# Kernel tuning notes

Measured on AMD Instinct MI355X. Metric: run time of the kernel, lower is better.

## Reference

```python
import jax, jax.numpy as jnp
import numpy as np

DIM, HEADS, MLP_HID = 1024, 16, 4096
B, N = 2, 2048
EPS = 1e-5

def setup_inputs() -> dict:
    key = jax.random.key(0)
    ks = jax.random.split(key, 8)
    s = lambda fan_in: 1.0 / np.sqrt(fan_in)
    return {
        "x": jax.random.normal(ks[0], (B, N, DIM), jnp.float32),
        "ln1_w": jnp.ones((DIM,), jnp.float32),
        "ln1_b": jnp.zeros((DIM,), jnp.float32),
        # weights stored [in, out] (transpose of torch Linear.weight)
        "qkv_w": jax.random.normal(ks[1], (DIM, 3 * DIM), jnp.float32) * s(DIM),
        "proj_w": jax.random.normal(ks[2], (DIM, DIM), jnp.float32) * s(DIM),
        "proj_b": jnp.zeros((DIM,), jnp.float32),
        "ln2_w": jnp.ones((DIM,), jnp.float32),
        "ln2_b": jnp.zeros((DIM,), jnp.float32),
        "fc1_w": jax.random.normal(ks[3], (DIM, MLP_HID), jnp.float32) * s(DIM),
        "fc1_b": jnp.zeros((MLP_HID,), jnp.float32),
        "fc2_w": jax.random.normal(ks[4], (MLP_HID, DIM), jnp.float32) * s(MLP_HID),
        "fc2_b": jnp.zeros((DIM,), jnp.float32),
    }

def _layernorm(x, w, b):
    mu = jnp.mean(x, axis=-1, keepdims=True)
    var = jnp.mean(jnp.square(x - mu), axis=-1, keepdims=True)
    return (x - mu) * jax.lax.rsqrt(var + EPS) * w + b

def reference(x, ln1_w, ln1_b, qkv_w, proj_w, proj_b, ln2_w, ln2_b, fc1_w, fc1_b, fc2_w, fc2_b):
    Bn, Nn, C = x.shape
    H, D = HEADS, C // HEADS
    scale = D ** -0.5

    # --- attention sub-block (pre-norm, residual) ---
    h = _layernorm(x, ln1_w, ln1_b)
    qkv = (h @ qkv_w).reshape(Bn, Nn, 3, H, D)
    q, k, v = jnp.moveaxis(qkv, 2, 0)  # each [B, N, H, D]
    attn = jnp.einsum('bnhd,bmhd->bhnm', q, k) * scale
    attn = jax.nn.softmax(attn, axis=-1)
    o = jnp.einsum('bhnm,bmhd->bnhd', attn, v).reshape(Bn, Nn, C)
    x = x + (o @ proj_w + proj_b)

    # --- MLP sub-block (pre-norm, residual) ---
    h = _layernorm(x, ln2_w, ln2_b)
    h = jax.nn.gelu(h @ fc1_w + fc1_b, approximate=False)
    x = x + (h @ fc2_w + fc2_b)
    return x
```

## Files before the change

kernel.cpp:

```cpp
#include <hip/hip_runtime.h>
#include <hip/hip_bf16.h>

typedef __attribute__((ext_vector_type(4))) float  f32x4;
typedef __attribute__((ext_vector_type(8))) short  short8;
typedef __attribute__((ext_vector_type(8))) unsigned short ushort8;
typedef __attribute__((ext_vector_type(4))) unsigned short u16x4;
typedef unsigned short u16;

__device__ __forceinline__ u16 f2bf(float f) {
    unsigned int u = __builtin_bit_cast(unsigned int, f);
    return (u16)((u + 0x7fffu + ((u >> 16) & 1u)) >> 16);
}

__device__ __forceinline__ unsigned cvtpk(float lo, float hi) {
    unsigned r;
    asm("v_cvt_pk_bf16_f32 %0, %1, %2" : "=v"(r) : "v"(lo), "v"(hi));
    return r;
}

__device__ __forceinline__ f32x4 mfma16(short8 a, short8 b, f32x4 c) {
    return __builtin_amdgcn_mfma_f32_16x16x32_bf16(a, b, c, 0, 0, 0);
}

__device__ __forceinline__ float fexp2(float x) {
    float r;
    asm("v_exp_f32 %0, %1" : "=v"(r) : "v"(x));
    return r;
}

__device__ __forceinline__ float fgelu(float v) {
    const float t = v * v;
    const float u = v * (-2.302118f - 0.102944f * t);
    return v / (1.0f + fexp2(u));
}

__device__ __forceinline__ void gload_lds16(const u16* g, u16* l) {
    __builtin_amdgcn_global_load_lds(
        (__attribute__((address_space(1))) void*)(uintptr_t)(g),
        (__attribute__((address_space(3))) void*)(unsigned)(uintptr_t)(l),
        16, 0, 0);
}

__device__ __forceinline__ void tcast_body(const float* __restrict__ W,
                                           u16* __restrict__ Wt,
                                           int K, int N, int bx, int by) {
    __shared__ float tile[32][33];
    const int tx = threadIdx.x & 31, ty = threadIdx.x >> 5;
    const int c0 = bx * 32;
    const int r0 = by * 32;
#pragma unroll
    for (int i = 0; i < 32; i += 8)
        tile[ty + i][tx] = W[(size_t)(r0 + ty + i) * N + c0 + tx];
    __syncthreads();
#pragma unroll
    for (int i = 0; i < 32; i += 8)
        Wt[(size_t)(c0 + ty + i) * K + r0 + tx] = f2bf(tile[tx][ty + i]);
}

__device__ __forceinline__ void ln_body(const float* __restrict__ x,
                                        const float* __restrict__ w,
                                        const float* __restrict__ b,
                                        u16* __restrict__ out, int row) {
    const int tid = threadIdx.x;
    const float4 v = ((const float4*)(x + (size_t)row * 1024))[tid];
    float s1 = v.x + v.y + v.z + v.w;
    float s2 = v.x * v.x + v.y * v.y + v.z * v.z + v.w * v.w;
#pragma unroll
    for (int m = 1; m < 64; m <<= 1) { s1 += __shfl_xor(s1, m); s2 += __shfl_xor(s2, m); }
    __shared__ float red1[4], red2[4];
    const int wave = tid >> 6, lane = tid & 63;
    if (lane == 0) { red1[wave] = s1; red2[wave] = s2; }
    __syncthreads();
    s1 = red1[0] + red1[1] + red1[2] + red1[3];
    s2 = red2[0] + red2[1] + red2[2] + red2[3];
    const float mean = s1 * (1.0f / 1024.0f);
    const float var  = s2 * (1.0f / 1024.0f) - mean * mean;
    const float rstd = rsqrtf(var + 1e-5f);
    const float4 wv = ((const float4*)w)[tid];
    const float4 bv = ((const float4*)b)[tid];
    u16x4 o;
    o[0] = f2bf((v.x - mean) * rstd * wv.x + bv.x);
    o[1] = f2bf((v.y - mean) * rstd * wv.y + bv.y);
    o[2] = f2bf((v.z - mean) * rstd * wv.z + bv.z);
    o[3] = f2bf((v.w - mean) * rstd * wv.w + bv.w);
    *(u16x4*)(out + (size_t)row * 1024 + tid * 4) = o;
}

__global__ __launch_bounds__(256) void prep_kernel(const float* __restrict__ x,
                                                   const float* __restrict__ ln1w,
                                                   const float* __restrict__ ln1b,
                                                   u16* __restrict__ h1,
                                                   const float* __restrict__ qkvw,
                                                   u16* __restrict__ wt_qkv,
                                                   const float* __restrict__ projw,
                                                   u16* __restrict__ wt_proj,
                                                   const float* __restrict__ fc1w,
                                                   u16* __restrict__ wt_fc1,
                                                   const float* __restrict__ fc2w,
                                                   u16* __restrict__ wt_fc2) {
    int id = blockIdx.x;
    if (id < 4096) { ln_body(x, ln1w, ln1b, h1, id); return; }
    id -= 4096;
    if (id < 3072) { tcast_body(qkvw, wt_qkv, 1024, 3072, id % 96, id / 96); return; }
    id -= 3072;
    if (id < 1024) { tcast_body(projw, wt_proj, 1024, 1024, id % 32, id / 32); return; }
    id -= 1024;
    if (id < 4096) { tcast_body(fc1w, wt_fc1, 1024, 4096, id % 128, id / 128); return; }
    id -= 4096;
    tcast_body(fc2w, wt_fc2, 4096, 1024, id % 32, id / 32);
}

__global__ __launch_bounds__(256) void ln_kernel(const float* __restrict__ x,
                                                 const float* __restrict__ w,
                                                 const float* __restrict__ b,
                                                 u16* __restrict__ out) {
    ln_body(x, w, b, out, blockIdx.x);
}

template <int HAS_BIAS, int HAS_RES, int DO_GELU, int OUT_BF16>
__global__ __launch_bounds__(512, 2) void gemm8_kernel(const u16* __restrict__ A,
                                                       const u16* __restrict__ Bt,
                                                       const float* __restrict__ bias,
                                                       const float* __restrict__ res,
                                                       void* __restrict__ Cout,
                                                       int M, int N, int K) {
    __shared__ __align__(16) u16 Ag[3][256 * 32];
    __shared__ __align__(16) u16 Bg[3][128 * 32];
    const int tid = threadIdx.x;
    const int wave = tid >> 6, lane = tid & 63;
    const int wr = wave >> 2, wc = wave & 3;
    const int fq = lane >> 4, fr = lane & 15;

    const int gx = gridDim.x;
    const int nwg = gx * gridDim.y;
    int bid = blockIdx.y * gx + blockIdx.x;
    bid = (bid & 7) * (nwg >> 3) + (bid >> 3);
    const size_t bm = (size_t)(bid / gx) * 256, bn = (size_t)(bid % gx) * 128;

    const int ko = (fq ^ ((fr >> 1) & 3)) * 8;

    const int srow = tid >> 2;
    const int scol = ((tid & 3) ^ ((tid >> 3) & 3)) * 8;
    const u16* Asrc = A  + (bm + srow) * (size_t)K + scol;
    const u16* Bsrc = Bt + (bn + srow) * (size_t)K + scol;
    const int sdst = wave * 512;

    f32x4 acc[8][2] = {};

    auto STAGE_G = [&](int slot, int kc) {
        gload_lds16(Asrc + kc,                      &Ag[slot][sdst]);
        gload_lds16(Asrc + (size_t)128 * K + kc,    &Ag[slot][sdst + 4096]);
        gload_lds16(Bsrc + kc,                      &Bg[slot][sdst]);
    };

    const int NG = K >> 5;
    STAGE_G(0, 0); STAGE_G(1, 32);
    asm volatile("s_waitcnt vmcnt(3)" ::: "memory");
    __builtin_amdgcn_s_barrier();

    int slot = 0;
    for (int g = 0; g < NG; g++) {
        short8 bfr[2], af[4];
#pragma unroll
        for (int nt = 0; nt < 2; nt++)
            bfr[nt] = *(const short8*)&Bg[slot][(wc * 32 + nt * 16 + fr) * 32 + ko];
#pragma unroll
        for (int m2 = 0; m2 < 4; m2++)
            af[m2] = *(const short8*)&Ag[slot][(wr * 128 + m2 * 16 + fr) * 32 + ko];
        if (g + 2 < NG) {
            const int s2 = slot >= 1 ? slot - 1 : slot + 2;
            STAGE_G(s2, (g + 2) * 32);
        }
        __builtin_amdgcn_s_barrier();
        __builtin_amdgcn_s_setprio(1);
#pragma unroll
        for (int m2 = 0; m2 < 4; m2++)
#pragma unroll
            for (int nt = 0; nt < 2; nt++)
                acc[m2][nt] = mfma16(af[m2], bfr[nt], acc[m2][nt]);
        __builtin_amdgcn_s_setprio(0);
        __builtin_amdgcn_s_barrier();
#pragma unroll
        for (int m2 = 0; m2 < 4; m2++)
            af[m2] = *(const short8*)&Ag[slot][(wr * 128 + (m2 + 4) * 16 + fr) * 32 + ko];
        __builtin_amdgcn_s_barrier();
        __builtin_amdgcn_s_setprio(1);
#pragma unroll
        for (int m2 = 0; m2 < 4; m2++)
#pragma unroll
            for (int nt = 0; nt < 2; nt++)
                acc[m2 + 4][nt] = mfma16(af[m2], bfr[nt], acc[m2 + 4][nt]);
        __builtin_amdgcn_s_setprio(0);
        if (g < NG - 2) { asm volatile("s_waitcnt vmcnt(3)" ::: "memory"); }
        else            { asm volatile("s_waitcnt vmcnt(0)" ::: "memory"); }
        __builtin_amdgcn_s_barrier();
        slot = slot == 2 ? 0 : slot + 1;
    }
#pragma unroll
    for (int mt = 0; mt < 8; mt++) {
#pragma unroll
        for (int nt = 0; nt < 2; nt++) {
            const size_t col = bn + wc * 32 + nt * 16 + fr;
            const float bb = HAS_BIAS ? bias[col] : 0.0f;
#pragma unroll
            for (int j = 0; j < 4; j++) {
                const size_t row = bm + wr * 128 + mt * 16 + fq * 4 + j;
                float v = acc[mt][nt][j] + bb;
                if (DO_GELU) v = fgelu(v);
                if (HAS_RES) v += res[row * N + col];
                if (OUT_BF16) ((u16*)Cout)[row * N + col] = f2bf(v);
                else          ((float*)Cout)[row * N + col] = v;
            }
        }
    }
}

template <int HAS_BIAS, int HAS_RES, int DO_GELU, int OUT_BF16>
__global__ __launch_bounds__(256) void gemm_kernel(const u16* __restrict__ A,
                                                   const u16* __restrict__ Bt,
                                                   const float* __restrict__ bias,
                                                   const float* __restrict__ res,
                                                   void* __restrict__ Cout,
                                                   int M, int N, int K) {
    __shared__ __align__(16) u16 As[2][128 * 64];
    __shared__ __align__(16) u16 Bs[2][128 * 64];
    const int tid = threadIdx.x;
    const int wave = tid >> 6, lane = tid & 63;
    const int wr = wave >> 1, wc = wave & 1;
    const int fq = lane >> 4, fr = lane & 15;

    const int gx = gridDim.x;
    const int nwg = gx * gridDim.y;
    int bid = blockIdx.y * gx + blockIdx.x;
    bid = (bid & 7) * (nwg >> 3) + (bid >> 3);
    const size_t bm = (size_t)(bid / gx) * 128, bn = (size_t)(bid % gx) * 128;

    const int lr = lane >> 3, seg = lane & 7;
    const int seg2 = seg ^ (lr & 7);

    const u16* Ab = A  + bm * (size_t)K + seg2 * 8;
    const u16* Bb = Bt + bn * (size_t)K + seg2 * 8;

    const int rx = fr & 7;
    const int ko0 = ((0 + fq) ^ rx) * 8;
    const int ko1 = ((4 + fq) ^ rx) * 8;

    f32x4 acc[4][4] = {};

    auto STAGE = [&](int buf, int k0) {
#pragma unroll
        for (int i = 0; i < 4; i++) {
            const int r = wave * 32 + i * 8 + lr;
            gload_lds16(Ab + (size_t)r * K + k0, &As[buf][(wave * 4 + i) * 512]);
            gload_lds16(Bb + (size_t)r * K + k0, &Bs[buf][(wave * 4 + i) * 512]);
        }
    };

    STAGE(0, 0);
    __syncthreads();
    int cur = 0;

    for (int k0 = 0; k0 < K; k0 += 64) {
        if (k0 + 64 < K) STAGE(cur ^ 1, k0 + 64);
#pragma unroll
        for (int ks = 0; ks < 2; ks++) {
            const int ko = ks ? ko1 : ko0;
            short8 af[4], bf[4];
#pragma unroll
            for (int t = 0; t < 4; t++) {
                af[t] = *(const short8*)&As[cur][(wr * 64 + t * 16 + fr) * 64 + ko];
                bf[t] = *(const short8*)&Bs[cur][(wc * 64 + t * 16 + fr) * 64 + ko];
            }
#pragma unroll
            for (int mt = 0; mt < 4; mt++)
#pragma unroll
                for (int nt = 0; nt < 4; nt++)
                    acc[mt][nt] = mfma16(af[mt], bf[nt], acc[mt][nt]);
        }
        __syncthreads();
        cur ^= 1;
    }
#pragma unroll
    for (int mt = 0; mt < 4; mt++) {
#pragma unroll
        for (int nt = 0; nt < 4; nt++) {
            const size_t col = bn + wc * 64 + nt * 16 + fr;
            const float bb = HAS_BIAS ? bias[col] : 0.0f;
#pragma unroll
            for (int j = 0; j < 4; j++) {
                const size_t row = bm + wr * 64 + mt * 16 + fq * 4 + j;
                float v = acc[mt][nt][j] + bb;
                if (DO_GELU) v = fgelu(v);
                if (HAS_RES) v += res[row * N + col];
                if (OUT_BF16) ((u16*)Cout)[row * N + col] = f2bf(v);
                else          ((float*)Cout)[row * N + col] = v;
            }
        }
    }
}

__global__ __launch_bounds__(512) void attn_kernel(const u16* __restrict__ qkv,
                                                   u16* __restrict__ O) {
    const int bh = blockIdx.x;
    const int b = bh >> 4, h = bh & 15;
    const int qb = blockIdx.y;
    const int tid = threadIdx.x, wave = tid >> 6, lane = tid & 63;
    const int fq = lane >> 4, fr = lane & 15;
    __shared__ __align__(16) u16 Ks[2][64 * 64];
    __shared__ __align__(16) u16 Vt[2][64 * 64];
    __shared__ __align__(16) u16 Pl[8][16 * 64];

    const size_t base = (size_t)b * 2048 * 3072;
    const int q0 = qb * 128 + wave * 16;

    short8 qf[2];
#pragma unroll
    for (int ks = 0; ks < 2; ks++)
        qf[ks] = *(const short8*)(qkv + base + (size_t)(q0 + fr) * 3072 + h * 64 + ks * 32 + fq * 8);

    const u16* kp = qkv + base + 1024 + (size_t)h * 64;
    const u16* vp = qkv + base + 2048 + (size_t)h * 64;
    const int krow = tid >> 3, kseg = tid & 7;
    const int kpos = (kseg ^ (krow & 7)) * 8;
    const int vkey = tid & 63, vdc = tid >> 6;

    const int rx = fr & 7;
    const int ko0 = ((0 + fq) ^ rx) * 8;
    const int ko1 = ((4 + fq) ^ rx) * 8;

    f32x4 accO[4] = {};
    float lq = 0.0f;

    const float c = 0.125f * 1.44269504f;

    ushort8 kreg = *(const ushort8*)(kp + (size_t)krow * 3072 + kseg * 8);
    ushort8 vreg = *(const ushort8*)(vp + (size_t)vkey * 3072 + vdc * 8);
    *(ushort8*)&Ks[0][krow * 64 + kpos] = kreg;
#pragma unroll
    for (int j = 0; j < 8; j++) {
        const int row = vdc * 8 + j;
        Vt[0][row * 64 + ((vkey >> 3) ^ (row & 7)) * 8 + (vkey & 7)] = vreg[j];
    }
    __syncthreads();
    int cur = 0;

    for (int kt = 0; kt < 32; kt++) {
        if (kt < 31) {
            kreg = *(const ushort8*)(kp + (size_t)((kt + 1) * 64 + krow) * 3072 + kseg * 8);
            vreg = *(const ushort8*)(vp + (size_t)((kt + 1) * 64 + vkey) * 3072 + vdc * 8);
        }
        f32x4 s[4];
#pragma unroll
        for (int nt = 0; nt < 4; nt++) {
            f32x4 a = {};
            short8 kf0 = *(const short8*)&Ks[cur][(nt * 16 + fr) * 64 + ko0];
            short8 kf1 = *(const short8*)&Ks[cur][(nt * 16 + fr) * 64 + ko1];
            a = mfma16(kf0, qf[0], a);
            a = mfma16(kf1, qf[1], a);
            s[nt] = a;
        }
#pragma unroll
        for (int nt = 0; nt < 4; nt++)
#pragma unroll
            for (int j = 0; j < 4; j++) {
                const float pij = fexp2(s[nt][j] * c);
                s[nt][j] = pij;
                lq += pij;
            }
#pragma unroll
        for (int nt = 0; nt < 4; nt++) {
            uint2 pw;
            pw.x = cvtpk(s[nt][0], s[nt][1]);
            pw.y = cvtpk(s[nt][2], s[nt][3]);
            const int chunk = nt * 2 + (fq >> 1);
            *(uint2*)&Pl[wave][fr * 64 + (chunk ^ rx) * 8 + (fq & 1) * 4] = pw;
        }
#pragma unroll
        for (int ks = 0; ks < 2; ks++) {
            const int ko = ks ? ko1 : ko0;
            short8 pf = *(const short8*)&Pl[wave][fr * 64 + ko];
#pragma unroll
            for (int dt = 0; dt < 4; dt++) {
                short8 vf = *(const short8*)&Vt[cur][(dt * 16 + fr) * 64 + ko];
                accO[dt] = mfma16(pf, vf, accO[dt]);
            }
        }
        if (kt < 31) {
            *(ushort8*)&Ks[cur ^ 1][krow * 64 + kpos] = kreg;
#pragma unroll
            for (int j = 0; j < 8; j++) {
                const int row = vdc * 8 + j;
                Vt[cur ^ 1][row * 64 + ((vkey >> 3) ^ (row & 7)) * 8 + (vkey & 7)] = vreg[j];
            }
        }
        __syncthreads();
        cur ^= 1;
    }
    lq += __shfl_xor(lq, 16);
    lq += __shfl_xor(lq, 32);
    float rq[4];
#pragma unroll
    for (int j = 0; j < 4; j++) rq[j] = 1.0f / __shfl(lq, fq * 4 + j);
#pragma unroll
    for (int dt = 0; dt < 4; dt++)
#pragma unroll
        for (int j = 0; j < 4; j++) {
            const float v = accO[dt][j] * rq[j];
            O[(size_t)(b * 2048 + q0 + fq * 4 + j) * 1024 + h * 64 + dt * 16 + fr] = f2bf(v);
        }
}

extern "C" void kernel_launch(void* const* d_in, const int* in_sizes, int n_in,
                              void* d_out, int out_size, void* d_ws, size_t ws_size,
                              hipStream_t stream) {
    (void)in_sizes; (void)n_in; (void)out_size; (void)ws_size;
    const float* x     = (const float*)d_in[0];
    const float* ln1w  = (const float*)d_in[1];
    const float* ln1b  = (const float*)d_in[2];
    const float* qkvw  = (const float*)d_in[3];
    const float* projw = (const float*)d_in[4];
    const float* projb = (const float*)d_in[5];
    const float* ln2w  = (const float*)d_in[6];
    const float* ln2b  = (const float*)d_in[7];
    const float* fc1w  = (const float*)d_in[8];
    const float* fc1b  = (const float*)d_in[9];
    const float* fc2w  = (const float*)d_in[10];
    const float* fc2b  = (const float*)d_in[11];

    char* p = (char*)d_ws;
    auto alloc = [&](size_t bytes) { void* r = p; p += (bytes + 255) & ~(size_t)255; return r; };
    u16* wt_qkv  = (u16*)alloc(3072ull * 1024 * 2);
    u16* wt_proj = (u16*)alloc(1024ull * 1024 * 2);
    u16* wt_fc1  = (u16*)alloc(4096ull * 1024 * 2);
    u16* wt_fc2  = (u16*)alloc(1024ull * 4096 * 2);
    u16* h1      = (u16*)alloc(4096ull * 1024 * 2);
    u16* qkv     = (u16*)alloc(4096ull * 3072 * 2);
    u16* attn_o  = (u16*)alloc(4096ull * 1024 * 2);
    u16* h2      = (u16*)alloc(4096ull * 1024 * 2);
    u16* mlp_h   = (u16*)alloc(4096ull * 4096 * 2);
    float* x1 = (float*)d_out;

    prep_kernel<<<16384, 256, 0, stream>>>(x, ln1w, ln1b, h1,
                                           qkvw, wt_qkv, projw, wt_proj,
                                           fc1w, wt_fc1, fc2w, wt_fc2);

    gemm8_kernel<0, 0, 0, 1><<<dim3(24, 16), 512, 0, stream>>>(h1, wt_qkv, nullptr, nullptr, qkv, 4096, 3072, 1024);
    attn_kernel<<<dim3(32, 16), 512, 0, stream>>>(qkv, attn_o);
    gemm_kernel<1, 1, 0, 0><<<dim3(8, 32), 256, 0, stream>>>(attn_o, wt_proj, projb, x, x1, 4096, 1024, 1024);

    ln_kernel<<<4096, 256, 0, stream>>>(x1, ln2w, ln2b, h2);
    gemm8_kernel<1, 0, 1, 1><<<dim3(32, 16), 512, 0, stream>>>(h2, wt_fc1, fc1b, nullptr, mlp_h, 4096, 4096, 1024);
    gemm_kernel<1, 1, 0, 0><<<dim3(8, 32), 256, 0, stream>>>(mlp_h, wt_fc2, fc2b, x1, d_out, 4096, 1024, 4096);
}
```

Before: 219.8 us.

## Overlap proj/fc1/fc2 weight cast-transpose with QKV GEMM in one launch

The prep kernel now only does LN1 and the QKV weight cast. The remaining weight transposes/casts (proj, fc1, fc2) are appended as extra blocks to a dedicated QKV GEMM kernel, so they run concurrently with the GEMM tiles. This aims to hide memory-bound transpose work behind compute-bound GEMM, at the cost of extra LDS for the tile and contention for CU slots. It relies on the 384 GEMM blocks being scheduled first.

```diff
diff --git a/kernel.cpp b/kernel.cpp
--- a/kernel.cpp
+++ b/kernel.cpp
@@ -86,28 +86,16 @@
     *(u16x4*)(out + (size_t)row * 1024 + tid * 4) = o;
 }
 
-__global__ __launch_bounds__(256) void prep_kernel(const float* __restrict__ x,
-                                                   const float* __restrict__ ln1w,
-                                                   const float* __restrict__ ln1b,
-                                                   u16* __restrict__ h1,
-                                                   const float* __restrict__ qkvw,
-                                                   u16* __restrict__ wt_qkv,
-                                                   const float* __restrict__ projw,
-                                                   u16* __restrict__ wt_proj,
-                                                   const float* __restrict__ fc1w,
-                                                   u16* __restrict__ wt_fc1,
-                                                   const float* __restrict__ fc2w,
-                                                   u16* __restrict__ wt_fc2) {
+__global__ __launch_bounds__(256) void prep1_kernel(const float* __restrict__ x,
+                                                    const float* __restrict__ ln1w,
+                                                    const float* __restrict__ ln1b,
+                                                    u16* __restrict__ h1,
+                                                    const float* __restrict__ qkvw,
+                                                    u16* __restrict__ wt_qkv) {
     int id = blockIdx.x;
     if (id < 4096) { ln_body(x, ln1w, ln1b, h1, id); return; }
     id -= 4096;
-    if (id < 3072) { tcast_body(qkvw, wt_qkv, 1024, 3072, id % 96, id / 96); return; }
-    id -= 3072;
-    if (id < 1024) { tcast_body(projw, wt_proj, 1024, 1024, id % 32, id / 32); return; }
-    id -= 1024;
-    if (id < 4096) { tcast_body(fc1w, wt_fc1, 1024, 4096, id % 128, id / 128); return; }
-    id -= 4096;
-    tcast_body(fc2w, wt_fc2, 4096, 1024, id % 32, id / 32);
+    tcast_body(qkvw, wt_qkv, 1024, 3072, id % 96, id / 96);
 }
 
 __global__ __launch_bounds__(256) void ln_kernel(const float* __restrict__ x,
@@ -115,6 +103,128 @@
                                                  const float* __restrict__ b,
                                                  u16* __restrict__ out) {
     ln_body(x, w, b, out, blockIdx.x);
+}
+
+__device__ __forceinline__ void tcast_body512(const float* __restrict__ W,
+                                              u16* __restrict__ Wt,
+                                              int K, int N, int bx, int by,
+                                              float (*tile)[33]) {
+    const int tx = threadIdx.x & 31, ty = threadIdx.x >> 5;
+    const int c0 = bx * 32;
+    const int r0 = by * 32;
+#pragma unroll
+    for (int i = 0; i < 32; i += 16)
+        tile[ty + i][tx] = W[(size_t)(r0 + ty + i) * N + c0 + tx];
+    __syncthreads();
+#pragma unroll
+    for (int i = 0; i < 32; i += 16)
+        Wt[(size_t)(c0 + ty + i) * K + r0 + tx] = f2bf(tile[tx][ty + i]);
+}
+
+__global__ __launch_bounds__(512, 2) void qkvfused_kernel(const u16* __restrict__ A,
+                                                          const u16* __restrict__ Bt,
+                                                          u16* __restrict__ Cout,
+                                                          const float* __restrict__ projw,
+                                                          u16* __restrict__ wt_proj,
+                                                          const float* __restrict__ fc1w,
+                                                          u16* __restrict__ wt_fc1,
+                                                          const float* __restrict__ fc2w,
+                                                          u16* __restrict__ wt_fc2) {
+    __shared__ __align__(16) u16 Ag[3][256 * 32];
+    __shared__ __align__(16) u16 Bg[3][128 * 32];
+    __shared__ float tile[32][33];
+    constexpr int K = 1024, N = 3072;
+
+    if (blockIdx.x >= 384) {
+        int id = blockIdx.x - 384;
+        if (id < 1024) { tcast_body512(projw, wt_proj, 1024, 1024, id % 32, id / 32, tile); return; }
+        id -= 1024;
+        if (id < 4096) { tcast_body512(fc1w, wt_fc1, 1024, 4096, id % 128, id / 128, tile); return; }
+        id -= 4096;
+        tcast_body512(fc2w, wt_fc2, 4096, 1024, id % 32, id / 32, tile);
+        return;
+    }
+
+    const int tid = threadIdx.x;
+    const int wave = tid >> 6, lane = tid & 63;
+    const int wr = wave >> 2, wc = wave & 3;
+    const int fq = lane >> 4, fr = lane & 15;
+
+    int bid = blockIdx.x;
+    bid = (bid & 7) * 48 + (bid >> 3);
+    const size_t bm = (size_t)(bid / 24) * 256, bn = (size_t)(bid % 24) * 128;
+
+    const int ko = (fq ^ ((fr >> 1) & 3)) * 8;
+
+    const int srow = tid >> 2;
+    const int scol = ((tid & 3) ^ ((tid >> 3) & 3)) * 8;
+    const u16* Asrc = A  + (bm + srow) * (size_t)K + scol;
+    const u16* Bsrc = Bt + (bn + srow) * (size_t)K + scol;
+    const int sdst = wave * 512;
+
+    f32x4 acc[8][2] = {};
+
+    auto STAGE_G = [&](int slot, int kc) {
+        gload_lds16(Asrc + kc,                      &Ag[slot][sdst]);
+        gload_lds16(Asrc + (size_t)128 * K + kc,    &Ag[slot][sdst + 4096]);
+        gload_lds16(Bsrc + kc,                      &Bg[slot][sdst]);
+    };
+
+    const int NG = K >> 5;
+    STAGE_G(0, 0); STAGE_G(1, 32);
+    asm volatile("s_waitcnt vmcnt(3)" ::: "memory");
+    __builtin_amdgcn_s_barrier();
+
+    int slot = 0;
+    for (int g = 0; g < NG; g++) {
+        short8 bfr[2], af[4];
+#pragma unroll
+        for (int nt = 0; nt < 2; nt++)
+            bfr[nt] = *(const short8*)&Bg[slot][(wc * 32 + nt * 16 + fr) * 32 + ko];
+#pragma unroll
+        for (int m2 = 0; m2 < 4; m2++)
+            af[m2] = *(const short8*)&Ag[slot][(wr * 128 + m2 * 16 + fr) * 32 + ko];
+        if (g + 2 < NG) {
+            const int s2 = slot >= 1 ? slot - 1 : slot + 2;
+            STAGE_G(s2, (g + 2) * 32);
+        }
+        __builtin_amdgcn_s_barrier();
+        __builtin_amdgcn_s_setprio(1);
+#pragma unroll
+        for (int m2 = 0; m2 < 4; m2++)
+#pragma unroll
+            for (int nt = 0; nt < 2; nt++)
+                acc[m2][nt] = mfma16(af[m2], bfr[nt], acc[m2][nt]);
+        __builtin_amdgcn_s_setprio(0);
+        __builtin_amdgcn_s_barrier();
+#pragma unroll
+        for (int m2 = 0; m2 < 4; m2++)
+            af[m2] = *(const short8*)&Ag[slot][(wr * 128 + (m2 + 4) * 16 + fr) * 32 + ko];
+        __builtin_amdgcn_s_barrier();
+        __builtin_amdgcn_s_setprio(1);
+#pragma unroll
+        for (int m2 = 0; m2 < 4; m2++)
+#pragma unroll
+            for (int nt = 0; nt < 2; nt++)
+                acc[m2 + 4][nt] = mfma16(af[m2], bfr[nt], acc[m2 + 4][nt]);
+        __builtin_amdgcn_s_setprio(0);
+        if (g < NG - 2) { asm volatile("s_waitcnt vmcnt(3)" ::: "memory"); }
+        else            { asm volatile("s_waitcnt vmcnt(0)" ::: "memory"); }
+        __builtin_amdgcn_s_barrier();
+        slot = slot == 2 ? 0 : slot + 1;
+    }
+#pragma unroll
+    for (int mt = 0; mt < 8; mt++) {
+#pragma unroll
+        for (int nt = 0; nt < 2; nt++) {
+            const size_t col = bn + wc * 32 + nt * 16 + fr;
+#pragma unroll
+            for (int j = 0; j < 4; j++) {
+                const size_t row = bm + wr * 128 + mt * 16 + fq * 4 + j;
+                Cout[row * N + col] = f2bf(acc[mt][nt][j]);
+            }
+        }
+    }
 }
 
 template <int HAS_BIAS, int HAS_RES, int DO_GELU, int OUT_BF16>
@@ -440,11 +550,11 @@
     u16* mlp_h   = (u16*)alloc(4096ull * 4096 * 2);
     float* x1 = (float*)d_out;
 
-    prep_kernel<<<16384, 256, 0, stream>>>(x, ln1w, ln1b, h1,
-                                           qkvw, wt_qkv, projw, wt_proj,
-                                           fc1w, wt_fc1, fc2w, wt_fc2);
-
-    gemm8_kernel<0, 0, 0, 1><<<dim3(24, 16), 512, 0, stream>>>(h1, wt_qkv, nullptr, nullptr, qkv, 4096, 3072, 1024);
+    prep1_kernel<<<7168, 256, 0, stream>>>(x, ln1w, ln1b, h1, qkvw, wt_qkv);
+
+    qkvfused_kernel<<<9600, 512, 0, stream>>>(h1, wt_qkv, qkv,
+                                              projw, wt_proj, fc1w, wt_fc1, fc2w, wt_fc2);
+
     attn_kernel<<<dim3(32, 16), 512, 0, stream>>>(qkv, attn_o);
     gemm_kernel<1, 1, 0, 0><<<dim3(8, 32), 256, 0, stream>>>(attn_o, wt_proj, projb, x, x1, 4096, 1024, 1024);
 
```

Result: no change. 217.8 us (-0.9%).
